# Kernel optimization log

Measured on AMD Instinct MI355X. Metric: run time of the kernel, lower is better.

The kernel has to match this reference:

```python
import jax, jax.numpy as jnp
import numpy as np

N, DIN, D, H, L, S, E = 3072, 64, 128, 4, 2, 4, 49152
NEG = -2.0**32 + 1.0


def _layernorm(x, g, b, eps=1e-5):
    m = jnp.mean(x, axis=-1, keepdims=True)
    v = jnp.var(x, axis=-1, keepdims=True)
    return (x - m) * jax.lax.rsqrt(v + eps) * g + b


def setup_inputs() -> dict:
    key = jax.random.key(0)
    ks = jax.random.split(key, 24)
    w = lambda k, shp: (0.02 * jax.random.normal(k, shp)).astype(jnp.float32)
    inp = {
        "x": jax.random.normal(ks[0], (N, DIN), dtype=jnp.float32),
        "edge_index": jax.random.randint(ks[1], (2, E), 0, N, dtype=jnp.int64) if jax.config.jax_enable_x64 else jax.random.randint(ks[1], (2, E), 0, N).astype(jnp.int32),
        "shortest_path_len": jax.random.randint(ks[2], (N, N), 0, 11).astype(jnp.int32),
        "edge_feat": jax.random.normal(ks[3], (N, N, S), dtype=jnp.float32),
        # input projection
        "node_W": w(ks[4], (DIN, D)), "node_b": jnp.zeros((D,), jnp.float32),
        # centrality / spatial / edge encodings
        "deg_emb": w(ks[5], (N, D)),
        "sp_emb": w(ks[6], (11, 1)),
        "edge_W": w(ks[7], (S, S)), "edge_b": jnp.zeros((S,), jnp.float32),
        # per-layer stacked attention params
        "ln1_g": jnp.ones((L, D), jnp.float32), "ln1_b": jnp.zeros((L, D), jnp.float32),
        "Wq": w(ks[8], (L, H, D, D)), "bq": jnp.zeros((L, H, D), jnp.float32),
        "Wk": w(ks[9], (L, H, D, D)), "bk": jnp.zeros((L, H, D), jnp.float32),
        "Wv": w(ks[10], (L, H, D, D)), "bv": jnp.zeros((L, H, D), jnp.float32),
        "Wo": w(ks[11], (L, H * D, D)), "bo": jnp.zeros((L, D), jnp.float32),
        "ln2_g": jnp.ones((L, D), jnp.float32), "ln2_b": jnp.zeros((L, D), jnp.float32),
        "ff_W": w(ks[12], (L, D, D)), "ff_b": jnp.zeros((L, D), jnp.float32),
        # output projection
        "out_W": w(ks[13], (D, D)), "out_b": jnp.zeros((D,), jnp.float32),
    }
    return inp


def reference(x, edge_index, shortest_path_len, edge_feat,
              node_W, node_b, deg_emb, sp_emb, edge_W, edge_b,
              ln1_g, ln1_b, Wq, bq, Wk, bk, Wv, bv, Wo, bo,
              ln2_g, ln2_b, ff_W, ff_b, out_W, out_b):
    # padding mask from raw features
    mask_idx = (jnp.sum(x, axis=1) != 0).astype(x.dtype)            # [N]
    mask = mask_idx[:, None] * mask_idx[None, :]                    # [N,N]

    h = x @ node_W + node_b                                         # [N,D]
    # centrality: degree of edge destinations
    deg = jax.ops.segment_sum(jnp.ones((edge_index.shape[1],), jnp.int32),
                              edge_index[1], num_segments=N)        # [N]
    h = h + deg_emb[deg]

    spatial = sp_emb[shortest_path_len][..., 0]                     # [N,N]
    edge_m = (edge_feat @ edge_W + edge_b).mean(axis=-1)            # [N,N]
    bias = spatial + edge_m
    scale = 1.0 / jnp.sqrt(jnp.asarray(D, x.dtype))

    for l in range(L):
        x_ln = _layernorm(h, ln1_g[l], ln1_b[l])                    # [N,D]
        q = jnp.einsum('nd,hdk->hnk', x_ln, Wq[l]) + bq[l][:, None, :]
        k = jnp.einsum('nd,hdk->hnk', x_ln, Wk[l]) + bk[l][:, None, :]
        v = jnp.einsum('nd,hdk->hnk', x_ln, Wv[l]) + bv[l][:, None, :]
        a = jnp.einsum('hnk,hmk->hnm', q, k) * scale + bias[None]   # [H,N,N]
        a = jnp.where(mask[None] == 0, NEG, a)
        s = jax.nn.softmax(a, axis=-1)
        s = jnp.where(mask[None] == 0, 0.0, s)
        o = jnp.einsum('hnm,hmd->hnd', s, v)                        # [H,N,D]
        cat = jnp.transpose(o, (1, 0, 2)).reshape(N, H * D)         # [N,H*D]
        x_out = cat @ Wo[l] + bo[l] + h
        h = _layernorm(x_out, ln2_g[l], ln2_b[l]) @ ff_W[l] + ff_b[l] + x_out

    return h @ out_W + out_b
```

## Files before the change

### kernel.cpp

```cpp
#include <hip/hip_runtime.h>
#include <math.h>

static constexpr int N   = 3072;
static constexpr int DIN = 64;
static constexpr int D   = 128;
static constexpr int H   = 4;
static constexpr int E   = 49152;
#define NEGV  (-4294967295.0f)
#define SCALE (0.08838834764831845f)

typedef unsigned short u16;
typedef __attribute__((ext_vector_type(8))) short short8;
typedef __attribute__((ext_vector_type(4))) float f32x4;
typedef __attribute__((ext_vector_type(4))) unsigned short u16x4;

__device__ __forceinline__ u16 f2bf(float f){
  unsigned int u = __float_as_uint(f);
  u += 0x7fff + ((u >> 16) & 1);
  return (u16)(u >> 16);
}
__device__ __forceinline__ float bf2f(u16 u){
  return __uint_as_float(((unsigned int)u) << 16);
}

__global__ void k_zero_deg(int* __restrict__ deg){
  int i = blockIdx.x*blockDim.x + threadIdx.x;
  if(i < N) deg[i] = 0;
}

__global__ void k_deg(const int* __restrict__ ei, int* __restrict__ deg){
  int e = blockIdx.x*blockDim.x + threadIdx.x;
  if(e < E) atomicAdd(&deg[ei[E + e]], 1);
}

__global__ void k_h0(const float* __restrict__ x, const float* __restrict__ nodeW,
                     const float* __restrict__ nodeb, const float* __restrict__ degemb,
                     const int* __restrict__ deg, const float* __restrict__ g1,
                     const float* __restrict__ b1, float* __restrict__ mask,
                     float* __restrict__ h, float* __restrict__ xln){
  const int i = blockIdx.x, t = threadIdx.x;
  float xv = x[i*DIN + t];
  float s = xv;
  #pragma unroll
  for(int o=32;o;o>>=1) s += __shfl_xor(s, o);
  if(t == 0) mask[i] = (s != 0.0f) ? 1.0f : 0.0f;
  __shared__ float xr[DIN];
  xr[t] = xv;
  __syncthreads();
  int dg = deg[i]; dg = dg > N-1 ? N-1 : dg;
  float a0 = nodeb[t]      + degemb[dg*D + t];
  float a1 = nodeb[t + 64] + degemb[dg*D + t + 64];
  #pragma unroll
  for(int u=0; u<DIN; ++u){
    float xu = xr[u];
    a0 = fmaf(xu, nodeW[u*D + t],      a0);
    a1 = fmaf(xu, nodeW[u*D + t + 64], a1);
  }
  h[i*D + t]      = a0;
  h[i*D + t + 64] = a1;
  float s2 = a0 + a1, sq = a0*a0 + a1*a1;
  #pragma unroll
  for(int o=32;o;o>>=1){ s2 += __shfl_xor(s2, o); sq += __shfl_xor(sq, o); }
  float mean = s2*(1.0f/128.0f);
  float var  = sq*(1.0f/128.0f) - mean*mean;
  float inv  = rsqrtf(var + 1e-5f);
  xln[i*D + t]      = (a0 - mean)*inv*g1[t]      + b1[t];
  xln[i*D + t + 64] = (a1 - mean)*inv*g1[t + 64] + b1[t + 64];
}

__global__ void k_bias(const int* __restrict__ spl, const float* __restrict__ ef,
                       const float* __restrict__ spe, const float* __restrict__ eW,
                       const float* __restrict__ eb, const float* __restrict__ mask,
                       u16* __restrict__ biasm){
  int idx = blockIdx.x*blockDim.x + threadIdx.x;
  int i = idx / N, j = idx % N;
  float wm0 = (eW[0] + eW[1] + eW[2] + eW[3])  * 0.25f;
  float wm1 = (eW[4] + eW[5] + eW[6] + eW[7])  * 0.25f;
  float wm2 = (eW[8] + eW[9] + eW[10]+ eW[11]) * 0.25f;
  float wm3 = (eW[12]+ eW[13]+ eW[14]+ eW[15]) * 0.25f;
  float bm  = (eb[0] + eb[1] + eb[2] + eb[3])  * 0.25f;
  float4 e4 = reinterpret_cast<const float4*>(ef)[idx];
  float em = fmaf(e4.x, wm0, fmaf(e4.y, wm1, fmaf(e4.z, wm2, fmaf(e4.w, wm3, bm))));
  float b = spe[spl[idx]] + em;
  float mk = mask[i]*mask[j];
  biasm[idx] = f2bf((mk != 0.0f) ? b : NEGV);
}

__global__ __launch_bounds__(256) void k_wt_all(const float* __restrict__ Wq, const float* __restrict__ Wk,
    const float* __restrict__ Wv, const float* __restrict__ ffW, const float* __restrict__ outW,
    u16* __restrict__ wt_qkv, u16* __restrict__ wt_ff, u16* __restrict__ wt_out){
  __shared__ float t[32][33];
  const int z = blockIdx.y;
  const float* src; u16* dst;
  if(z < 24){
    int l = z/12, r = z%12;
    const float* W = (r>>2)==0 ? Wq : (r>>2)==1 ? Wk : Wv;
    src = W + (size_t)(l*4 + (r&3))*16384;
    dst = wt_qkv + (size_t)z*16384;
  } else if(z < 26){
    src = ffW + (size_t)(z-24)*16384; dst = wt_ff + (size_t)(z-24)*16384;
  } else { src = outW; dst = wt_out; }
  const int ki = blockIdx.x & 3, ni = blockIdx.x >> 2;
  const int tid = threadIdx.x;
  #pragma unroll
  for(int i=0;i<4;i++){
    int idx = tid + i*256, r = idx>>5, c = idx&31;
    t[r][c] = src[(size_t)(ki*32+r)*128 + ni*32 + c];
  }
  __syncthreads();
  #pragma unroll
  for(int i=0;i<4;i++){
    int idx = tid + i*256, r = idx>>5, c = idx&31;
    dst[(size_t)(ni*32+r)*128 + ki*32 + c] = f2bf(t[c][r]);
  }
}

__global__ __launch_bounds__(256) void k_wt_wo(const float* __restrict__ Wo, u16* __restrict__ wt_wo){
  __shared__ float t[32][33];
  const int l = blockIdx.y;
  const float* src = Wo + (size_t)l*65536;
  u16* dst = wt_wo + (size_t)l*65536;
  const int ki = blockIdx.x & 15, ni = blockIdx.x >> 4;
  const int tid = threadIdx.x;
  #pragma unroll
  for(int i=0;i<4;i++){
    int idx = tid + i*256, r = idx>>5, c = idx&31;
    t[r][c] = src[(size_t)(ki*32+r)*128 + ni*32 + c];
  }
  __syncthreads();
  #pragma unroll
  for(int i=0;i<4;i++){
    int idx = tid + i*256, r = idx>>5, c = idx&31;
    dst[(size_t)(ni*32+r)*512 + ki*32 + c] = f2bf(t[c][r]);
  }
}

template<int MODE>
__device__ __forceinline__ void mgemm_body(const float* __restrict__ A, const u16* __restrict__ Bt,
                                           const float* __restrict__ bias, void* __restrict__ Cv){
  __shared__ u16 As[64*128];
  __shared__ u16 Bs[128*128];
  const int tid = threadIdx.x, w = tid>>6, lane = tid&63;
  const int g4 = lane>>4, l16 = lane&15;
  const int m0 = blockIdx.x*64;
  const int srow = tid>>4, sch = tid&15;
  f32x4 acc[8];
  #pragma unroll
  for(int nt=0;nt<8;++nt) acc[nt] = (f32x4){0.f,0.f,0.f,0.f};
  #pragma unroll
  for(int it=0;it<4;++it){
    int row = it*16 + srow;
    const float4* ap = reinterpret_cast<const float4*>(A + (size_t)(m0+row)*128 + sch*8);
    float4 x0 = ap[0], x1 = ap[1];
    u16x4 p0, p1;
    p0.x=f2bf(x0.x); p0.y=f2bf(x0.y); p0.z=f2bf(x0.z); p0.w=f2bf(x0.w);
    p1.x=f2bf(x1.x); p1.y=f2bf(x1.y); p1.z=f2bf(x1.z); p1.w=f2bf(x1.w);
    u16* dst = &As[row*128 + ((sch ^ (row&15))*8)];
    *reinterpret_cast<u16x4*>(dst)     = p0;
    *reinterpret_cast<u16x4*>(dst + 4) = p1;
  }
  #pragma unroll
  for(int it=0;it<8;++it){
    int row = it*16 + srow;
    short8 b = *reinterpret_cast<const short8*>(Bt + (size_t)row*128 + sch*8);
    *reinterpret_cast<short8*>(&Bs[row*128 + ((sch ^ (row&15))*8)]) = b;
  }
  __syncthreads();
  __builtin_amdgcn_s_setprio(1);
  #pragma unroll
  for(int c=0;c<4;++c){
    short8 af = *reinterpret_cast<const short8*>(&As[(w*16+l16)*128 + (((c*4+g4) ^ l16)*8)]);
    #pragma unroll
    for(int nt=0;nt<8;++nt){
      short8 bf = *reinterpret_cast<const short8*>(&Bs[(nt*16+l16)*128 + (((c*4+g4) ^ l16)*8)]);
      acc[nt] = __builtin_amdgcn_mfma_f32_16x16x32_bf16(af, bf, acc[nt], 0, 0, 0);
    }
  }
  __builtin_amdgcn_s_setprio(0);
  const int mrow = m0 + w*16 + g4*4;
  #pragma unroll
  for(int nt=0;nt<8;++nt){
    const int col = nt*16 + l16;
    float bi = bias[col];
    if(MODE == 2){
      u16x4 t;
      t.x = f2bf(acc[nt][0] + bi); t.y = f2bf(acc[nt][1] + bi);
      t.z = f2bf(acc[nt][2] + bi); t.w = f2bf(acc[nt][3] + bi);
      *reinterpret_cast<u16x4*>((u16*)Cv + (size_t)col*N + mrow) = t;
    } else {
      #pragma unroll
      for(int rg=0;rg<4;++rg){
        float v = acc[nt][rg] + bi;
        if(MODE == 1) ((u16*)Cv)[(size_t)(mrow+rg)*128 + col] = f2bf(v);
        else          ((float*)Cv)[(size_t)(mrow+rg)*128 + col] = v;
      }
    }
  }
}

__global__ __launch_bounds__(256) void k_mqkv(const float* __restrict__ xln, const u16* __restrict__ wt_qkv,
    const float* __restrict__ bq, const float* __restrict__ bk, const float* __restrict__ bv,
    u16* __restrict__ q, u16* __restrict__ k, u16* __restrict__ vT, int l){
  const int z = blockIdx.y, which = z>>2, head = z&3;
  const u16* Bt = wt_qkv + (size_t)(l*12 + z)*16384;
  if(which == 0)      mgemm_body<1>(xln, Bt, bq + (l*H+head)*D, q  + (size_t)head*N*D);
  else if(which == 1) mgemm_body<1>(xln, Bt, bk + (l*H+head)*D, k  + (size_t)head*N*D);
  else                mgemm_body<2>(xln, Bt, bv + (l*H+head)*D, vT + (size_t)head*N*D);
}

__global__ __launch_bounds__(256) void k_mout(const float* __restrict__ h, const u16* __restrict__ wt_out,
    const float* __restrict__ outb, float* __restrict__ out){
  mgemm_body<0>(h, wt_out, outb, out);
}

template<int S>
__global__ __launch_bounds__(256) void k_mwo(const float* __restrict__ opart, const float* __restrict__ mpart,
    const float* __restrict__ lpart, const float* __restrict__ mask, const u16* __restrict__ wt,
    const float* __restrict__ bo, const float* __restrict__ hres,
    float* __restrict__ xout, float* __restrict__ xln,
    const float* __restrict__ g2, const float* __restrict__ b2){
  __shared__ u16 As[64*128];
  __shared__ u16 Bs[128*128];
  const int tid = threadIdx.x, w = tid>>6, lane = tid&63;
  const int g4 = lane>>4, l16 = lane&15;
  const int m0 = blockIdx.x*64;
  const int srow = tid>>4, sch = tid&15;
  f32x4 acc[8];
  #pragma unroll
  for(int nt=0;nt<8;++nt) acc[nt] = (f32x4){0.f,0.f,0.f,0.f};
  for(int k0 = 0; k0 < 512; k0 += 128){
    const int hh = k0 >> 7;
    __syncthreads();
    #pragma unroll
    for(int it=0;it<4;++it){
      int row = it*16 + srow;
      int grow = m0 + row;
      float w_[S]; float M = -INFINITY; float mv[S], lv[S];
      #pragma unroll
      for(int s=0;s<S;++s){
        mv[s] = mpart[(size_t)(s*H + hh)*N + grow];
        lv[s] = lpart[(size_t)(s*H + hh)*N + grow];
        M = fmaxf(M, mv[s]);
      }
      float denom = 0.f;
      #pragma unroll
      for(int s=0;s<S;++s){ w_[s] = __expf(mv[s] - M); denom = fmaf(lv[s], w_[s], denom); }
      float scale = mask[grow] / denom;
      const int d = sch*8;
      float4 v0 = make_float4(0,0,0,0), v1 = make_float4(0,0,0,0);
      #pragma unroll
      for(int s=0;s<S;++s){
        const float4* op = reinterpret_cast<const float4*>(
            opart + ((size_t)(s*H + hh)*N + grow)*D + d);
        float4 a = op[0], b = op[1];
        v0.x = fmaf(a.x, w_[s], v0.x); v0.y = fmaf(a.y, w_[s], v0.y);
        v0.z = fmaf(a.z, w_[s], v0.z); v0.w = fmaf(a.w, w_[s], v0.w);
        v1.x = fmaf(b.x, w_[s], v1.x); v1.y = fmaf(b.y, w_[s], v1.y);
        v1.z = fmaf(b.z, w_[s], v1.z); v1.w = fmaf(b.w, w_[s], v1.w);
      }
      u16x4 p0, p1;
      p0.x=f2bf(v0.x*scale); p0.y=f2bf(v0.y*scale); p0.z=f2bf(v0.z*scale); p0.w=f2bf(v0.w*scale);
      p1.x=f2bf(v1.x*scale); p1.y=f2bf(v1.y*scale); p1.z=f2bf(v1.z*scale); p1.w=f2bf(v1.w*scale);
      u16* dst = &As[row*128 + ((sch ^ (row&15))*8)];
      *reinterpret_cast<u16x4*>(dst)     = p0;
      *reinterpret_cast<u16x4*>(dst + 4) = p1;
    }
    #pragma unroll
    for(int it=0;it<8;++it){
      int row = it*16 + srow;
      short8 b = *reinterpret_cast<const short8*>(wt + (size_t)row*512 + k0 + sch*8);
      *reinterpret_cast<short8*>(&Bs[row*128 + ((sch ^ (row&15))*8)]) = b;
    }
    __syncthreads();
    __builtin_amdgcn_s_setprio(1);
    #pragma unroll
    for(int c=0;c<4;++c){
      short8 af = *reinterpret_cast<const short8*>(&As[(w*16+l16)*128 + (((c*4+g4) ^ l16)*8)]);
      #pragma unroll
      for(int nt=0;nt<8;++nt){
        short8 bf = *reinterpret_cast<const short8*>(&Bs[(nt*16+l16)*128 + (((c*4+g4) ^ l16)*8)]);
        acc[nt] = __builtin_amdgcn_mfma_f32_16x16x32_bf16(af, bf, acc[nt], 0, 0, 0);
      }
    }
    __builtin_amdgcn_s_setprio(0);
  }
  const int mrow = m0 + w*16 + g4*4;
  float s_[4] = {0,0,0,0}, q_[4] = {0,0,0,0};
  #pragma unroll
  for(int nt=0;nt<8;++nt){
    const int col = nt*16 + l16;
    float bi = bo[col];
    #pragma unroll
    for(int rg=0;rg<4;++rg){
      float v = acc[nt][rg] + bi + hres[(size_t)(mrow+rg)*128 + col];
      acc[nt][rg] = v;
      s_[rg] += v; q_[rg] = fmaf(v, v, q_[rg]);
    }
  }
  #pragma unroll
  for(int o=1;o<16;o<<=1){
    #pragma unroll
    for(int rg=0;rg<4;++rg){ s_[rg] += __shfl_xor(s_[rg], o); q_[rg] += __shfl_xor(q_[rg], o); }
  }
  float mean[4], inv[4];
  #pragma unroll
  for(int rg=0;rg<4;++rg){
    mean[rg] = s_[rg]*(1.0f/128.0f);
    float var = q_[rg]*(1.0f/128.0f) - mean[rg]*mean[rg];
    inv[rg] = rsqrtf(var + 1e-5f);
  }
  #pragma unroll
  for(int nt=0;nt<8;++nt){
    const int col = nt*16 + l16;
    float gg = g2[col], bb = b2[col];
    #pragma unroll
    for(int rg=0;rg<4;++rg){
      float v = acc[nt][rg];
      xout[(size_t)(mrow+rg)*128 + col] = v;
      xln [(size_t)(mrow+rg)*128 + col] = (v - mean[rg])*inv[rg]*gg + bb;
    }
  }
}

__global__ __launch_bounds__(256) void k_mff(const float* __restrict__ xlnin, const u16* __restrict__ wt,
    const float* __restrict__ ffb, const float* __restrict__ res, float* __restrict__ hout,
    float* __restrict__ xlnout, const float* __restrict__ g1n, const float* __restrict__ b1n,
    int write_ln){
  __shared__ u16 As[64*128];
  __shared__ u16 Bs[128*128];
  const int tid = threadIdx.x, w = tid>>6, lane = tid&63;
  const int g4 = lane>>4, l16 = lane&15;
  const int m0 = blockIdx.x*64;
  const int srow = tid>>4, sch = tid&15;
  f32x4 acc[8];
  #pragma unroll
  for(int nt=0;nt<8;++nt) acc[nt] = (f32x4){0.f,0.f,0.f,0.f};
  #pragma unroll
  for(int it=0;it<4;++it){
    int row = it*16 + srow;
    const float4* ap = reinterpret_cast<const float4*>(xlnin + (size_t)(m0+row)*128 + sch*8);
    float4 x0 = ap[0], x1 = ap[1];
    u16x4 p0, p1;
    p0.x=f2bf(x0.x); p0.y=f2bf(x0.y); p0.z=f2bf(x0.z); p0.w=f2bf(x0.w);
    p1.x=f2bf(x1.x); p1.y=f2bf(x1.y); p1.z=f2bf(x1.z); p1.w=f2bf(x1.w);
    u16* dst = &As[row*128 + ((sch ^ (row&15))*8)];
    *reinterpret_cast<u16x4*>(dst)     = p0;
    *reinterpret_cast<u16x4*>(dst + 4) = p1;
  }
  #pragma unroll
  for(int it=0;it<8;++it){
    int row = it*16 + srow;
    short8 b = *reinterpret_cast<const short8*>(wt + (size_t)row*128 + sch*8);
    *reinterpret_cast<short8*>(&Bs[row*128 + ((sch ^ (row&15))*8)]) = b;
  }
  __syncthreads();
  __builtin_amdgcn_s_setprio(1);
  #pragma unroll
  for(int c=0;c<4;++c){
    short8 af = *reinterpret_cast<const short8*>(&As[(w*16+l16)*128 + (((c*4+g4) ^ l16)*8)]);
    #pragma unroll
    for(int nt=0;nt<8;++nt){
      short8 bf = *reinterpret_cast<const short8*>(&Bs[(nt*16+l16)*128 + (((c*4+g4) ^ l16)*8)]);
      acc[nt] = __builtin_amdgcn_mfma_f32_16x16x32_bf16(af, bf, acc[nt], 0, 0, 0);
    }
  }
  __builtin_amdgcn_s_setprio(0);
  const int mrow = m0 + w*16 + g4*4;
  float s_[4] = {0,0,0,0}, q_[4] = {0,0,0,0};
  #pragma unroll
  for(int nt=0;nt<8;++nt){
    const int col = nt*16 + l16;
    float bi = ffb[col];
    #pragma unroll
    for(int rg=0;rg<4;++rg){
      float v = acc[nt][rg] + bi + res[(size_t)(mrow+rg)*128 + col];
      acc[nt][rg] = v;
      s_[rg] += v; q_[rg] = fmaf(v, v, q_[rg]);
    }
  }
  #pragma unroll
  for(int nt=0;nt<8;++nt){
    const int col = nt*16 + l16;
    #pragma unroll
    for(int rg=0;rg<4;++rg)
      hout[(size_t)(mrow+rg)*128 + col] = acc[nt][rg];
  }
  if(write_ln){
    #pragma unroll
    for(int o=1;o<16;o<<=1){
      #pragma unroll
      for(int rg=0;rg<4;++rg){ s_[rg] += __shfl_xor(s_[rg], o); q_[rg] += __shfl_xor(q_[rg], o); }
    }
    #pragma unroll
    for(int rg=0;rg<4;++rg){
      float mean = s_[rg]*(1.0f/128.0f);
      float var  = q_[rg]*(1.0f/128.0f) - mean*mean;
      float inv  = rsqrtf(var + 1e-5f);
      s_[rg] = mean; q_[rg] = inv;
    }
    #pragma unroll
    for(int nt=0;nt<8;++nt){
      const int col = nt*16 + l16;
      float gg = g1n[col], bb = b1n[col];
      #pragma unroll
      for(int rg=0;rg<4;++rg)
        xlnout[(size_t)(mrow+rg)*128 + col] = (acc[nt][rg] - s_[rg])*q_[rg]*gg + bb;
    }
  }
}

__global__ __launch_bounds__(256) void k_attn(const u16* __restrict__ q, const u16* __restrict__ k,
                     const u16* __restrict__ vT, const u16* __restrict__ biasm,
                     float* __restrict__ opart, float* __restrict__ mpart, float* __restrict__ lpart,
                     int kvlen){
  const int tid  = threadIdx.x;
  const int w    = tid >> 6;
  const int lane = tid & 63;
  const int g4 = lane >> 4, l16 = lane & 15;
  const int head = blockIdx.y, sp = blockIdx.z;
  const int r0 = blockIdx.x*64 + w*16;
  __shared__ u16 Ks[64*128];
  __shared__ u16 Vs[64*128];
  __shared__ u16 P[4][16][40];

  const u16* qbase = q + ((size_t)head*N + r0)*D;
  short8 qf[4];
  #pragma unroll
  for(int c=0;c<4;c++)
    qf[c] = *reinterpret_cast<const short8*>(qbase + l16*D + c*32 + g4*8);

  f32x4 o[8];
  #pragma unroll
  for(int dt=0;dt<8;dt++) o[dt] = (f32x4){0.f,0.f,0.f,0.f};
  float m = -INFINITY, lsum = 0.0f;

  const u16* kh   = k  + (size_t)head*N*D;
  const u16* vTh  = vT + (size_t)head*D*N;
  const u16* brow = biasm + (size_t)(r0 + l16)*N;
  const int kv0 = sp*kvlen;

  const int krow = tid >> 4, kch = tid & 15;
  const int vrow = tid >> 3, vch = tid & 7;

  short8 kreg[4], vreg[4]; u16x4 bb[4];
  #pragma unroll
  for(int it=0; it<4; ++it)
    kreg[it] = *reinterpret_cast<const short8*>(kh + (size_t)(kv0 + it*16 + krow)*D + kch*8);
  #pragma unroll
  for(int it=0; it<4; ++it)
    vreg[it] = *reinterpret_cast<const short8*>(vTh + (size_t)(it*32 + vrow)*N + kv0 + vch*8);
  #pragma unroll
  for(int z=0; z<4; ++z)
    bb[z] = *reinterpret_cast<const u16x4*>(brow + kv0 + z*16 + g4*4);

  for(int j0 = kv0; j0 < kv0 + kvlen; j0 += 64){
    const int jn = (j0 + 64 < kv0 + kvlen) ? j0 + 64 : kv0;
    __syncthreads();
    #pragma unroll
    for(int it=0; it<4; ++it){
      int row = it*16 + krow;
      *reinterpret_cast<short8*>(&Ks[row*128 + ((kch ^ (row&15))*8)]) = kreg[it];
    }
    #pragma unroll
    for(int it=0; it<4; ++it){
      int d = it*32 + vrow;
      int row = d & 63, ch = ((d>>6)<<3) | vch;
      *reinterpret_cast<short8*>(&Vs[row*128 + ((ch ^ (row&15))*8)]) = vreg[it];
    }
    __syncthreads();

    short8 kreg2[4], vreg2[4]; u16x4 bb2[4];
    #pragma unroll
    for(int it=0; it<4; ++it)
      kreg2[it] = *reinterpret_cast<const short8*>(kh + (size_t)(jn + it*16 + krow)*D + kch*8);
    #pragma unroll
    for(int it=0; it<4; ++it)
      vreg2[it] = *reinterpret_cast<const short8*>(vTh + (size_t)(it*32 + vrow)*N + jn + vch*8);
    #pragma unroll
    for(int z=0; z<4; ++z)
      bb2[z] = *reinterpret_cast<const u16x4*>(brow + jn + z*16 + g4*4);

    #pragma unroll
    for(int ks=0; ks<2; ++ks){
      short8 kf[8];
      const int rowA = ks*32 + l16, rowB = rowA + 16;
      #pragma unroll
      for(int c=0;c<4;c++){
        kf[c]   = *reinterpret_cast<const short8*>(&Ks[rowA*128 + (((c*4+g4) ^ l16)*8)]);
        kf[4+c] = *reinterpret_cast<const short8*>(&Ks[rowB*128 + (((c*4+g4) ^ l16)*8)]);
      }
      f32x4 sA = (f32x4){0.f,0.f,0.f,0.f}, sB = sA;
      __builtin_amdgcn_s_setprio(1);
      #pragma unroll
      for(int c=0;c<4;c++){
        sA = __builtin_amdgcn_mfma_f32_16x16x32_bf16(kf[c],   qf[c], sA, 0, 0, 0);
        sB = __builtin_amdgcn_mfma_f32_16x16x32_bf16(kf[4+c], qf[c], sB, 0, 0, 0);
      }
      __builtin_amdgcn_s_setprio(0);
      u16x4 bA = bb[2*ks], bB = bb[2*ks+1];
      sA[0] = fmaf(sA[0], SCALE, bf2f(bA.x)); sA[1] = fmaf(sA[1], SCALE, bf2f(bA.y));
      sA[2] = fmaf(sA[2], SCALE, bf2f(bA.z)); sA[3] = fmaf(sA[3], SCALE, bf2f(bA.w));
      sB[0] = fmaf(sB[0], SCALE, bf2f(bB.x)); sB[1] = fmaf(sB[1], SCALE, bf2f(bB.y));
      sB[2] = fmaf(sB[2], SCALE, bf2f(bB.z)); sB[3] = fmaf(sB[3], SCALE, bf2f(bB.w));
      float pmax = fmaxf(fmaxf(fmaxf(sA[0],sA[1]), fmaxf(sA[2],sA[3])),
                         fmaxf(fmaxf(sB[0],sB[1]), fmaxf(sB[2],sB[3])));
      pmax = fmaxf(pmax, __shfl_xor(pmax, 16));
      pmax = fmaxf(pmax, __shfl_xor(pmax, 32));
      if(!__all(pmax - m <= 8.0f)){
        float mnew = fmaxf(m, pmax);
        float corr = __expf(m - mnew);
        lsum *= corr;
        float c0 = __shfl(corr, (lane & 48) | (g4*4 + 0));
        float c1 = __shfl(corr, (lane & 48) | (g4*4 + 1));
        float c2 = __shfl(corr, (lane & 48) | (g4*4 + 2));
        float c3 = __shfl(corr, (lane & 48) | (g4*4 + 3));
        #pragma unroll
        for(int dt=0;dt<8;dt++){
          o[dt][0] *= c0; o[dt][1] *= c1; o[dt][2] *= c2; o[dt][3] *= c3;
        }
        m = mnew;
      }
      f32x4 pA, pB;
      #pragma unroll
      for(int rg=0;rg<4;rg++){ pA[rg] = __expf(sA[rg] - m); pB[rg] = __expf(sB[rg] - m); }
      float ps = (pA[0]+pA[1]) + (pA[2]+pA[3]) + ((pB[0]+pB[1]) + (pB[2]+pB[3]));
      ps += __shfl_xor(ps, 16);
      ps += __shfl_xor(ps, 32);
      lsum += ps;
      u16x4 wa, wb;
      wa.x = f2bf(pA[0]); wa.y = f2bf(pA[1]); wa.z = f2bf(pA[2]); wa.w = f2bf(pA[3]);
      wb.x = f2bf(pB[0]); wb.y = f2bf(pB[1]); wb.z = f2bf(pB[2]); wb.w = f2bf(pB[3]);
      *reinterpret_cast<u16x4*>(&P[w][l16][g4*4])      = wa;
      *reinterpret_cast<u16x4*>(&P[w][l16][16 + g4*4]) = wb;
      short8 pf = *reinterpret_cast<const short8*>(&P[w][l16][g4*8]);
      __builtin_amdgcn_s_setprio(1);
      #pragma unroll
      for(int dt=0;dt<8;dt++){
        int d = dt*16 + l16;
        int row = d & 63;
        int ch  = ((dt>>2)<<3) | (ks<<2) | g4;
        short8 vf = *reinterpret_cast<const short8*>(&Vs[row*128 + ((ch ^ l16)*8)]);
        o[dt] = __builtin_amdgcn_mfma_f32_16x16x32_bf16(pf, vf, o[dt], 0, 0, 0);
      }
      __builtin_amdgcn_s_setprio(0);
    }
    #pragma unroll
    for(int it=0; it<4; ++it){ kreg[it] = kreg2[it]; vreg[it] = vreg2[it]; }
    #pragma unroll
    for(int z=0; z<4; ++z) bb[z] = bb2[z];
  }

  float* ob = opart + ((size_t)((sp*H + head)*N) + r0)*D;
  #pragma unroll
  for(int dt=0;dt<8;dt++){
    #pragma unroll
    for(int rg=0;rg<4;rg++)
      ob[(size_t)(g4*4+rg)*D + dt*16 + l16] = o[dt][rg];
  }
  if(g4 == 0){
    mpart[(size_t)(sp*H + head)*N + r0 + l16] = m;
    lpart[(size_t)(sp*H + head)*N + r0 + l16] = lsum;
  }
}

extern "C" void kernel_launch(void* const* d_in, const int* in_sizes, int n_in,
                              void* d_out, int out_size, void* d_ws, size_t ws_size,
                              hipStream_t stream){
  const float* x      = (const float*)d_in[0];
  const int*   ei     = (const int*)  d_in[1];
  const int*   spl    = (const int*)  d_in[2];
  const float* ef     = (const float*)d_in[3];
  const float* nodeW  = (const float*)d_in[4];
  const float* nodeb  = (const float*)d_in[5];
  const float* degemb = (const float*)d_in[6];
  const float* spe    = (const float*)d_in[7];
  const float* eW     = (const float*)d_in[8];
  const float* eb     = (const float*)d_in[9];
  const float* ln1g   = (const float*)d_in[10];
  const float* ln1b   = (const float*)d_in[11];
  const float* Wq     = (const float*)d_in[12];
  const float* bq     = (const float*)d_in[13];
  const float* Wk     = (const float*)d_in[14];
  const float* bk     = (const float*)d_in[15];
  const float* Wv     = (const float*)d_in[16];
  const float* bv     = (const float*)d_in[17];
  const float* Wo     = (const float*)d_in[18];
  const float* bo     = (const float*)d_in[19];
  const float* ln2g   = (const float*)d_in[20];
  const float* ln2b   = (const float*)d_in[21];
  const float* ffW    = (const float*)d_in[22];
  const float* ffb    = (const float*)d_in[23];
  const float* outW   = (const float*)d_in[24];
  const float* outb   = (const float*)d_in[25];

  constexpr size_t WT_ELEMS = 24*16384 + 2*16384 + 16384 + 2*65536;
  auto needed = [](int s)->size_t{
    size_t fl = 8192 + 3*(size_t)N*D;
    size_t bf = 3*(size_t)H*N*D + (size_t)N*N;
    size_t pf = (size_t)s*H*N*D + 2*(size_t)s*H*N;
    return fl*4 + bf*2 + pf*4 + WT_ELEMS*2;
  };
  int S = 2;
  if(needed(4) <= ws_size) S = 4;

  float* ws   = (float*)d_ws;
  int*   deg  = (int*)ws;
  float* mask = ws + 4096;
  float* h    = ws + 8192;
  float* xln  = h    + N*D;
  float* xout = xln  + N*D;
  u16*   qb   = (u16*)(xout + N*D);
  u16*   kb   = qb + (size_t)H*N*D;
  u16*   vTb  = kb + (size_t)H*N*D;
  u16*   biasm= vTb + (size_t)H*N*D;
  float* opart= (float*)(biasm + (size_t)N*N);
  float* mpart= opart + (size_t)S*H*N*D;
  float* lpart= mpart + (size_t)S*H*N;
  u16*   wt_qkv = (u16*)(lpart + (size_t)S*H*N);
  u16*   wt_ff  = wt_qkv + 24*16384;
  u16*   wt_out = wt_ff  + 2*16384;
  u16*   wt_wo  = wt_out + 16384;

  k_wt_all<<<dim3(16, 27), 256, 0, stream>>>(Wq, Wk, Wv, ffW, outW, wt_qkv, wt_ff, wt_out);
  k_wt_wo<<<dim3(64, 2), 256, 0, stream>>>(Wo, wt_wo);
  k_zero_deg<<<(N+255)/256, 256, 0, stream>>>(deg);
  k_deg<<<(E+255)/256, 256, 0, stream>>>(ei, deg);
  k_h0<<<N, 64, 0, stream>>>(x, nodeW, nodeb, degemb, deg, ln1g, ln1b, mask, h, xln);
  k_bias<<<(N*N)/256, 256, 0, stream>>>(spl, ef, spe, eW, eb, mask, biasm);

  for(int l = 0; l < 2; ++l){
    k_mqkv<<<dim3(N/64, 12), 256, 0, stream>>>(xln, wt_qkv, bq, bk, bv, qb, kb, vTb, l);
    k_attn<<<dim3(N/64, H, S), 256, 0, stream>>>(qb, kb, vTb, biasm, opart, mpart, lpart, N/S);
    if(S == 4)
      k_mwo<4><<<N/64, 256, 0, stream>>>(opart, mpart, lpart, mask, wt_wo + (size_t)l*65536,
                                         bo + l*D, h, xout, xln, ln2g + l*D, ln2b + l*D);
    else
      k_mwo<2><<<N/64, 256, 0, stream>>>(opart, mpart, lpart, mask, wt_wo + (size_t)l*65536,
                                         bo + l*D, h, xout, xln, ln2g + l*D, ln2b + l*D);
    k_mff<<<N/64, 256, 0, stream>>>(xln, wt_ff + (size_t)l*16384, ffb + l*D, xout, h, xln,
                                    ln1g + (l==0 ? D : 0), ln1b + (l==0 ? D : 0), l==0 ? 1 : 0);
  }
  k_mout<<<N/64, 256, 0, stream>>>(h, wt_out, outb, (float*)d_out);
}
```

Baseline: 265.3 us.

## Stage V-transpose stores through LDS and drop register prefetch in attention

The QKV GEMM's transposed-V epilogue now writes its tile into shared memory first, then issues coalesced 16-byte row stores to global memory instead of scattered 8-byte column writes. The attention kernel no longer prefetches the next K/V/bias tile into a second register set during compute. It loads each tile at the top of the iteration instead, which lowers register pressure and may raise occupancy. The cost is exposed global load latency before each tile's LDS store, plus two extra barriers in the GEMM epilogue.

```diff
diff --git a/kernel.cpp b/kernel.cpp
--- a/kernel.cpp
+++ b/kernel.cpp
@@ -178,16 +178,31 @@
   }
   __builtin_amdgcn_s_setprio(0);
   const int mrow = m0 + w*16 + g4*4;
-  #pragma unroll
-  for(int nt=0;nt<8;++nt){
-    const int col = nt*16 + l16;
-    float bi = bias[col];
-    if(MODE == 2){
+  if(MODE == 2){
+    __syncthreads();
+    u16* T = Bs;
+    #pragma unroll
+    for(int nt=0;nt<8;++nt){
+      const int col = nt*16 + l16;
+      float bi = bias[col];
       u16x4 t;
       t.x = f2bf(acc[nt][0] + bi); t.y = f2bf(acc[nt][1] + bi);
       t.z = f2bf(acc[nt][2] + bi); t.w = f2bf(acc[nt][3] + bi);
-      *reinterpret_cast<u16x4*>((u16*)Cv + (size_t)col*N + mrow) = t;
-    } else {
+      *reinterpret_cast<u16x4*>(&T[col*68 + (w*16 + g4*4)]) = t;
+    }
+    __syncthreads();
+    #pragma unroll
+    for(int i=0;i<4;++i){
+      int slot = tid + i*256;
+      int col = slot >> 3, q = slot & 7;
+      short8 v = *reinterpret_cast<const short8*>(&T[col*68 + q*8]);
+      *reinterpret_cast<short8*>((u16*)Cv + (size_t)col*N + m0 + q*8) = v;
+    }
+  } else {
+    #pragma unroll
+    for(int nt=0;nt<8;++nt){
+      const int col = nt*16 + l16;
+      float bi = bias[col];
       #pragma unroll
       for(int rg=0;rg<4;++rg){
         float v = acc[nt][rg] + bi;
@@ -442,19 +457,19 @@
   const int krow = tid >> 4, kch = tid & 15;
   const int vrow = tid >> 3, vch = tid & 7;
 
-  short8 kreg[4], vreg[4]; u16x4 bb[4];
-  #pragma unroll
-  for(int it=0; it<4; ++it)
-    kreg[it] = *reinterpret_cast<const short8*>(kh + (size_t)(kv0 + it*16 + krow)*D + kch*8);
-  #pragma unroll
-  for(int it=0; it<4; ++it)
-    vreg[it] = *reinterpret_cast<const short8*>(vTh + (size_t)(it*32 + vrow)*N + kv0 + vch*8);
-  #pragma unroll
-  for(int z=0; z<4; ++z)
-    bb[z] = *reinterpret_cast<const u16x4*>(brow + kv0 + z*16 + g4*4);
-
   for(int j0 = kv0; j0 < kv0 + kvlen; j0 += 64){
-    const int jn = (j0 + 64 < kv0 + kvlen) ? j0 + 64 : kv0;
+    short8 kreg[4], vreg[4];
+    #pragma unroll
+    for(int it=0; it<4; ++it)
+      kreg[it] = *reinterpret_cast<const short8*>(kh + (size_t)(j0 + it*16 + krow)*D + kch*8);
+    #pragma unroll
+    for(int it=0; it<4; ++it)
+      vreg[it] = *reinterpret_cast<const short8*>(vTh + (size_t)(it*32 + vrow)*N + j0 + vch*8);
+    u16x4 bb[4];
+    #pragma unroll
+    for(int z=0; z<4; ++z)
+      bb[z] = *reinterpret_cast<const u16x4*>(brow + j0 + z*16 + g4*4);
+
     __syncthreads();
     #pragma unroll
     for(int it=0; it<4; ++it){
@@ -468,17 +483,6 @@
       *reinterpret_cast<short8*>(&Vs[row*128 + ((ch ^ (row&15))*8)]) = vreg[it];
     }
     __syncthreads();
-
-    short8 kreg2[4], vreg2[4]; u16x4 bb2[4];
-    #pragma unroll
-    for(int it=0; it<4; ++it)
-      kreg2[it] = *reinterpret_cast<const short8*>(kh + (size_t)(jn + it*16 + krow)*D + kch*8);
-    #pragma unroll
-    for(int it=0; it<4; ++it)
-      vreg2[it] = *reinterpret_cast<const short8*>(vTh + (size_t)(it*32 + vrow)*N + jn + vch*8);
-    #pragma unroll
-    for(int z=0; z<4; ++z)
-      bb2[z] = *reinterpret_cast<const u16x4*>(brow + jn + z*16 + g4*4);
 
     #pragma unroll
     for(int ks=0; ks<2; ++ks){
@@ -544,10 +548,6 @@
       }
       __builtin_amdgcn_s_setprio(0);
     }
-    #pragma unroll
-    for(int it=0; it<4; ++it){ kreg[it] = kreg2[it]; vreg[it] = vreg2[it]; }
-    #pragma unroll
-    for(int z=0; z<4; ++z) bb[z] = bb2[z];
   }
 
   float* ob = opart + ((size_t)((sp*H + head)*N) + r0)*D;
```

Result: faster. 242.3 us (-8.7%).
